# Kernel tuning notes

Measured on AMD Instinct MI355X. Metric: run time of the kernel, lower is better.

The kernel has to match this reference:

```python
import jax, jax.numpy as jnp
import numpy as np

N = 200000
MUL = 64
# e3nn normalization (irrep_normalization='component', path_normalization='element'):
# FCTP(irreps, '1x0e', irreps): per-out-irrep norm sqrt(dim)/sqrt(num_elements) * w3j(l,0,l)=1/sqrt(dim)
#   -> overall 1/sqrt(mul_in)
INV_SQRT_MUL = 1.0 / np.sqrt(MUL)        # lin0 / sc : single path, fan-in 64
INV_SQRT_2MUL = 1.0 / np.sqrt(2 * MUL)   # final lin : two mid paths feed each output irrep (fan-in 128)
INV_SQRT3 = 1.0 / np.sqrt(3.0)           # w3j(1,1,0) dot-product CG coefficient


def setup_inputs() -> dict:
    key = jax.random.key(0)
    ks = jax.random.split(key, 12)
    f = lambda k, s: jax.random.normal(k, s, dtype=jnp.float32)
    return {
        'x1': f(ks[0], (N, 4 * MUL)),          # node feats: 64x0e + 64x1o
        'edge_attr': f(ks[1], (N, 4)),         # 1x0e + 1x1o spherical harmonics
        'tp_weight': f(ks[2], (N, 4 * MUL)),   # external uvu weights, 4 paths x 64
        'node_attr': f(ks[3], (N, 1)),         # 1x0e scalar attrs
        'W_lin0_s': f(ks[4], (MUL, MUL)),
        'W_lin0_v': f(ks[5], (MUL, MUL)),
        'W_sc_s': f(ks[6], (MUL, MUL)),
        'W_sc_v': f(ks[7], (MUL, MUL)),
        'W_lin_A': f(ks[8], (MUL, MUL)),
        'W_lin_D': f(ks[9], (MUL, MUL)),
        'W_lin_B': f(ks[10], (MUL, MUL)),
        'W_lin_C': f(ks[11], (MUL, MUL)),
    }


def _fctp_scalar_attr(s, v, a, Ws, Wv, c):
    # FullyConnectedTensorProduct(mul x {0e,1o}, 1x0e, mul x {0e,1o}) with scalar attr a: [N,1]
    out_s = c * a * (s @ Ws)                                   # [N,64]
    out_v = c * a[:, :, None] * jnp.einsum('num,uw->nwm', v, Wv)  # [N,64,3]
    return out_s, out_v


def reference(x1, edge_attr, tp_weight, node_attr,
              W_lin0_s, W_lin0_v, W_sc_s, W_sc_v,
              W_lin_A, W_lin_D, W_lin_B, W_lin_C):
    n = x1.shape[0]
    s = x1[:, :MUL]                     # 64x0e
    v = x1[:, MUL:].reshape(n, MUL, 3)  # 64x1o
    a = node_attr                       # [N,1]
    e0 = edge_attr[:, :1]               # 1x0e
    e1 = edge_attr[:, 1:4]              # 1x1o

    # self-connection and input linear (both FCTP with scalar node attrs)
    sc_s, sc_v = _fctp_scalar_attr(s, v, a, W_sc_s, W_sc_v, INV_SQRT_MUL)
    s0, v0 = _fctp_scalar_attr(s, v, a, W_lin0_s, W_lin0_v, INV_SQRT_MUL)

    # uvu TensorProduct with external per-element weights; instruction order A,B,C,D
    wA = tp_weight[:, 0:MUL]
    wB = tp_weight[:, MUL:2 * MUL]
    wC = tp_weight[:, 2 * MUL:3 * MUL]
    wD = tp_weight[:, 3 * MUL:4 * MUL]
    midA = wA * s0 * e0                                              # 0e x 0e -> 0e
    midB = wB[:, :, None] * s0[:, :, None] * e1[:, None, :]         # 0e x 1o -> 1o
    midC = wC[:, :, None] * v0 * e0[:, :, None]                     # 1o x 0e -> 1o
    midD = INV_SQRT3 * wD * jnp.einsum('num,nm->nu', v0, e1)        # 1o x 1o -> 0e (dot)
    # dropout (e3nn irrep dropout) in eval mode == identity

    # final FCTP(irreps_mid, 1x0e, irreps_out): two mid paths per output irrep
    out_s = INV_SQRT_2MUL * a * (midA @ W_lin_A + midD @ W_lin_D)
    out_v = INV_SQRT_2MUL * a[:, :, None] * (
        jnp.einsum('num,uw->nwm', midB, W_lin_B)
        + jnp.einsum('num,uw->nwm', midC, W_lin_C))

    out_s = out_s + sc_s
    out_v = out_v + sc_v
    return jnp.concatenate([out_s, out_v.reshape(n, 3 * MUL)], axis=1)
```

## Files before the change

kernel.cpp:

```cpp
#include <hip/hip_runtime.h>

typedef __attribute__((ext_vector_type(4))) float f32x4;
typedef __attribute__((ext_vector_type(8))) short bf16x8;

#define MFMA(a, b, c) __builtin_amdgcn_mfma_f32_16x16x32_bf16(a, b, c, 0, 0, 0)
#define NOPS asm volatile("s_nop 7\ns_nop 7\ns_nop 7\ns_nop 7" ::: "memory")

static __device__ __forceinline__ short rnebf(float x) {
  union { float f; unsigned u; } v; v.f = x;
  return (short)((v.u + 0x7FFFu + ((v.u >> 16) & 1u)) >> 16);
}
static __device__ __forceinline__ float bf2f(short h) {
  union { unsigned u; float f; } v; v.u = ((unsigned)(unsigned short)h) << 16;
  return v.f;
}
static __device__ __forceinline__ void split2(float x, short& hi, short& lo) {
  hi = rnebf(x);
  lo = rnebf(x - bf2f(hi));
}

__global__ void prep_w(const float* __restrict__ W0, const float* __restrict__ W1,
                       const float* __restrict__ W2, const float* __restrict__ W3,
                       const float* __restrict__ W4, const float* __restrict__ W5,
                       const float* __restrict__ W6, const float* __restrict__ W7,
                       short* __restrict__ ws) {
  const float* W[8] = {W0, W1, W2, W3, W4, W5, W6, W7};
  int t = blockIdx.x * 256 + threadIdx.x;
  int lane = t & 63, fragid = (t >> 6) & 7, mat = t >> 9;
  const float* Wm = W[mat];
  int ct = fragid >> 1, kh = fragid & 1;
  int wcol = ct * 16 + (lane & 15);
  int k0 = kh * 32 + ((lane >> 4) << 3);
  bf16x8 vh, vl;
#pragma unroll
  for (int j = 0; j < 8; ++j) {
    short h, l;
    split2(Wm[(k0 + j) * 64 + wcol], h, l);
    vh[j] = h; vl[j] = l;
  }
  size_t base = ((size_t)(mat * 16) + fragid) * 512 + lane * 8;
  *(bf16x8*)(ws + base) = vh;
  *(bf16x8*)(ws + base + 4096) = vl;
}

struct BF { bf16x8 h[4][2], l[4][2]; };

static __device__ __forceinline__ void loadB(const short* __restrict__ ws, int mat, int lane,
                                             BF& B) {
#pragma unroll
  for (int ct = 0; ct < 4; ++ct)
#pragma unroll
    for (int kh = 0; kh < 2; ++kh) {
      B.h[ct][kh] = *(const bf16x8*)(ws + ((size_t)(mat * 16) + ct * 2 + kh) * 512 + lane * 8);
      B.l[ct][kh] = *(const bf16x8*)(ws + ((size_t)(mat * 16 + 8) + ct * 2 + kh) * 512 + lane * 8);
    }
}

static __device__ __forceinline__ void cluster(const bf16x8 (&ah)[2], const bf16x8 (&al)[2],
                                               const BF& B, f32x4 (&acc)[4]) {
  __builtin_amdgcn_sched_barrier(0);
#pragma unroll
  for (int ct = 0; ct < 4; ++ct)
#pragma unroll
    for (int kh = 0; kh < 2; ++kh) {
      acc[ct] = MFMA(ah[kh], B.h[ct][kh], acc[ct]);
      acc[ct] = MFMA(al[kh], B.h[ct][kh], acc[ct]);
      acc[ct] = MFMA(ah[kh], B.l[ct][kh], acc[ct]);
    }
  __builtin_amdgcn_sched_barrier(0);
  NOPS;
}

static __device__ __forceinline__ void ldM(const short* __restrict__ M, int ph, int arow,
                                           int lane, bf16x8 (&ah)[2], bf16x8 (&al)[2]) {
  int swz = (arow & 7) << 4;
#pragma unroll
  for (int kh = 0; kh < 2; ++kh) {
    int ab = (arow * 128 + kh * 64 + ((lane >> 4) << 4)) ^ swz;
    ah[kh] = *(const bf16x8*)((const char*)M + ph * 8192 + ab);
    al[kh] = *(const bf16x8*)((const char*)M + (ph + 1) * 8192 + ab);
  }
}
static __device__ __forceinline__ void stM(short* __restrict__ M, int p, int n, int w, float x) {
  short h, l;
  split2(x, h, l);
  int ab = (n * 128 + w * 2) ^ ((n & 7) << 4);
  *(short*)((char*)M + p * 8192 + ab) = h;
  *(short*)((char*)M + (p + 1) * 8192 + ab) = l;
}

__global__ __launch_bounds__(256, 2) void fused_tp(
    const float* __restrict__ x1, const float* __restrict__ edge,
    const float* __restrict__ tp, const float* __restrict__ node,
    const short* __restrict__ ws, float* __restrict__ out) {
  __shared__ short lds_s[8 * 4096];
  __shared__ float cst[64 * 6];
  const int t = threadIdx.x;
  const int R0 = blockIdx.x * 64;

  {
    int c = t;
    int plane_hi, u;
    if (c < 64) { plane_hi = 0; u = c; }
    else { int q = c - 64; u = q / 3; int m = q - u * 3; plane_hi = 2 + 2 * m; }
    char* phi = (char*)lds_s + plane_hi * 8192;
    char* plo = phi + 8192;
    const float* xc = x1 + (size_t)R0 * 256 + c;
#pragma unroll 8
    for (int i = 0; i < 64; ++i) {
      float ksc = 0.125f * node[R0 + i];
      short h, l;
      split2(ksc * xc[(size_t)i * 256], h, l);
      int ab = (i * 128 + u * 2) ^ ((i & 7) << 4);
      *(short*)(phi + ab) = h;
      *(short*)(plo + ab) = l;
    }
    if (t < 64) {
      f32x4 e = *(const f32x4*)(edge + (size_t)(R0 + t) * 4);
      float a = node[R0 + t];
      float* cr = cst + t * 6;
      cr[0] = e[0]; cr[1] = e[1]; cr[2] = e[2]; cr[3] = e[3];
      cr[4] = 0.08838834764831845f * a;
    }
  }
  __syncthreads();

  const int lane = t & 63;
  const int wid = t >> 6;
  const int r0 = wid * 16;
  const int lg = lane >> 4;
  const int arow = r0 + (lane & 15);
  const f32x4 z = {0.f, 0.f, 0.f, 0.f};

  f32x4 outS[4], outV[3][4], s0v[4], v0v[3][4];
#pragma unroll
  for (int ct = 0; ct < 4; ++ct) { outS[ct] = z; s0v[ct] = z; }
#pragma unroll
  for (int m = 0; m < 3; ++m)
#pragma unroll
    for (int ct = 0; ct < 4; ++ct) { outV[m][ct] = z; v0v[m][ct] = z; }

  {
    BF B;
    bf16x8 ah[2], al[2];
    loadB(ws, 0, lane, B);
    ldM(lds_s, 0, arow, lane, ah, al);
    cluster(ah, al, B, outS);
    loadB(ws, 1, lane, B);
    cluster(ah, al, B, s0v);
    loadB(ws, 2, lane, B);
#pragma unroll
    for (int m = 0; m < 3; ++m) {
      ldM(lds_s, 2 + 2 * m, arow, lane, ah, al);
      cluster(ah, al, B, outV[m]);
    }
    loadB(ws, 3, lane, B);
#pragma unroll
    for (int m = 0; m < 3; ++m) {
      ldM(lds_s, 2 + 2 * m, arow, lane, ah, al);
      cluster(ah, al, B, v0v[m]);
    }
  }
  __syncthreads();

#pragma unroll
  for (int reg = 0; reg < 4; ++reg) {
    int n = r0 + (lg << 2) + reg;
    const float* cr = cst + n * 6;
    float e0 = cr[0], e1x = cr[1], e1y = cr[2], e1z = cr[3], c2a = cr[4];
    const float* tr = tp + (size_t)(R0 + n) * 256;
#pragma unroll
    for (int ct = 0; ct < 4; ++ct) {
      int w = ct * 16 + (lane & 15);
      float t0 = c2a * s0v[ct][reg];
      float wa = tr[w], wb = tr[64 + w];
      stM(lds_s, 0, n, w, wa * t0 * e0);
      float bmul = wb * t0;
      stM(lds_s, 2, n, w, bmul * e1x);
      stM(lds_s, 4, n, w, bmul * e1y);
      stM(lds_s, 6, n, w, bmul * e1z);
    }
  }
  __syncthreads();

  {
    BF B;
    bf16x8 ah[2], al[2];
    loadB(ws, 4, lane, B);
    ldM(lds_s, 0, arow, lane, ah, al);
    cluster(ah, al, B, outS);
    loadB(ws, 6, lane, B);
#pragma unroll
    for (int m = 0; m < 3; ++m) {
      ldM(lds_s, 2 + 2 * m, arow, lane, ah, al);
      cluster(ah, al, B, outV[m]);
    }
  }
  __syncthreads();

#pragma unroll
  for (int reg = 0; reg < 4; ++reg) {
    int n = r0 + (lg << 2) + reg;
    const float* cr = cst + n * 6;
    float e0 = cr[0], e1x = cr[1], e1y = cr[2], e1z = cr[3], c2a = cr[4];
    const float* tr = tp + (size_t)(R0 + n) * 256;
#pragma unroll
    for (int ct = 0; ct < 4; ++ct) {
      int w = ct * 16 + (lane & 15);
      float kv0 = c2a * v0v[0][ct][reg];
      float kv1 = c2a * v0v[1][ct][reg];
      float kv2 = c2a * v0v[2][ct][reg];
      float wc = tr[128 + w], wd = tr[192 + w];
      stM(lds_s, 0, n, w, wd * (kv0 * e1x + kv1 * e1y + kv2 * e1z) * 0.5773502691896258f);
      stM(lds_s, 2, n, w, wc * kv0 * e0);
      stM(lds_s, 4, n, w, wc * kv1 * e0);
      stM(lds_s, 6, n, w, wc * kv2 * e0);
    }
  }
  __syncthreads();

  {
    BF B;
    bf16x8 ah[2], al[2];
    loadB(ws, 5, lane, B);
    ldM(lds_s, 0, arow, lane, ah, al);
    cluster(ah, al, B, outS);
    loadB(ws, 7, lane, B);
#pragma unroll
    for (int m = 0; m < 3; ++m) {
      ldM(lds_s, 2 + 2 * m, arow, lane, ah, al);
      cluster(ah, al, B, outV[m]);
    }
  }

#pragma unroll
  for (int reg = 0; reg < 4; ++reg) {
    int n = r0 + (lg << 2) + reg;
    float* orow = out + (size_t)(R0 + n) * 256;
#pragma unroll
    for (int ct = 0; ct < 4; ++ct) {
      int w = ct * 16 + (lane & 15);
      orow[w] = outS[ct][reg];
      float* vp = orow + 64 + 3 * w;
      vp[0] = outV[0][ct][reg];
      vp[1] = outV[1][ct][reg];
      vp[2] = outV[2][ct][reg];
    }
  }
}

extern "C" void kernel_launch(void* const* d_in, const int* in_sizes, int n_in,
                              void* d_out, int out_size, void* d_ws, size_t ws_size,
                              hipStream_t stream) {
  const float* x1   = (const float*)d_in[0];
  const float* edge = (const float*)d_in[1];
  const float* tp   = (const float*)d_in[2];
  const float* node = (const float*)d_in[3];
  short* ws = (short*)d_ws;
  int n = in_sizes[0] / 256;

  prep_w<<<16, 256, 0, stream>>>(
      (const float*)d_in[6], (const float*)d_in[4],
      (const float*)d_in[7], (const float*)d_in[5],
      (const float*)d_in[8], (const float*)d_in[9],
      (const float*)d_in[10], (const float*)d_in[11], ws);

  fused_tp<<<n / 64, 256, 0, stream>>>(x1, edge, tp, node, ws, (float*)d_out);
}
```

Baseline: 202.1 us.

## Split output columns across two waves per row tile with 512-thread blocks

Doubles the block to 512 threads, so each 16-row tile is handled by two waves that each compute half of the 64 output columns. Per-wave accumulator and B-fragment register footprints are halved, which could allow more waves in flight, and the initial LDS staging loop is split between the two thread halves. The cost is that every A fragment is now loaded from LDS by twice as many waves. Each wave also has shorter MFMA clusters relative to the fixed NOP padding and barrier overhead.

```diff
diff --git a/kernel.cpp b/kernel.cpp
--- a/kernel.cpp
+++ b/kernel.cpp
@@ -43,29 +43,30 @@
   *(bf16x8*)(ws + base + 4096) = vl;
 }
 
-struct BF { bf16x8 h[4][2], l[4][2]; };
+struct BF2 { bf16x8 h[2][2], l[2][2]; };
 
 static __device__ __forceinline__ void loadB(const short* __restrict__ ws, int mat, int lane,
-                                             BF& B) {
-#pragma unroll
-  for (int ct = 0; ct < 4; ++ct)
+                                             int ch, BF2& B) {
+#pragma unroll
+  for (int cti = 0; cti < 2; ++cti)
 #pragma unroll
     for (int kh = 0; kh < 2; ++kh) {
-      B.h[ct][kh] = *(const bf16x8*)(ws + ((size_t)(mat * 16) + ct * 2 + kh) * 512 + lane * 8);
-      B.l[ct][kh] = *(const bf16x8*)(ws + ((size_t)(mat * 16 + 8) + ct * 2 + kh) * 512 + lane * 8);
+      int ct = 2 * ch + cti;
+      B.h[cti][kh] = *(const bf16x8*)(ws + ((size_t)(mat * 16) + ct * 2 + kh) * 512 + lane * 8);
+      B.l[cti][kh] = *(const bf16x8*)(ws + ((size_t)(mat * 16 + 8) + ct * 2 + kh) * 512 + lane * 8);
     }
 }
 
 static __device__ __forceinline__ void cluster(const bf16x8 (&ah)[2], const bf16x8 (&al)[2],
-                                               const BF& B, f32x4 (&acc)[4]) {
+                                               const BF2& B, f32x4 (&acc)[2]) {
   __builtin_amdgcn_sched_barrier(0);
 #pragma unroll
-  for (int ct = 0; ct < 4; ++ct)
+  for (int cti = 0; cti < 2; ++cti)
 #pragma unroll
     for (int kh = 0; kh < 2; ++kh) {
-      acc[ct] = MFMA(ah[kh], B.h[ct][kh], acc[ct]);
-      acc[ct] = MFMA(al[kh], B.h[ct][kh], acc[ct]);
-      acc[ct] = MFMA(ah[kh], B.l[ct][kh], acc[ct]);
+      acc[cti] = MFMA(ah[kh], B.h[cti][kh], acc[cti]);
+      acc[cti] = MFMA(al[kh], B.h[cti][kh], acc[cti]);
+      acc[cti] = MFMA(ah[kh], B.l[cti][kh], acc[cti]);
     }
   __builtin_amdgcn_sched_barrier(0);
   NOPS;
@@ -89,7 +90,7 @@
   *(short*)((char*)M + (p + 1) * 8192 + ab) = l;
 }
 
-__global__ __launch_bounds__(256, 2) void fused_tp(
+__global__ __launch_bounds__(512, 2) void fused_tp(
     const float* __restrict__ x1, const float* __restrict__ edge,
     const float* __restrict__ tp, const float* __restrict__ node,
     const short* __restrict__ ws, float* __restrict__ out) {
@@ -97,9 +98,11 @@
   __shared__ float cst[64 * 6];
   const int t = threadIdx.x;
   const int R0 = blockIdx.x * 64;
-
-  {
-    int c = t;
+  const int lane = t & 63;
+
+  {
+    int c = t & 255;
+    int half = t >> 8;
     int plane_hi, u;
     if (c < 64) { plane_hi = 0; u = c; }
     else { int q = c - 64; u = q / 3; int m = q - u * 3; plane_hi = 2 + 2 * m; }
@@ -107,7 +110,8 @@
     char* plo = phi + 8192;
     const float* xc = x1 + (size_t)R0 * 256 + c;
 #pragma unroll 8
-    for (int i = 0; i < 64; ++i) {
+    for (int ii = 0; ii < 32; ++ii) {
+      int i = half * 32 + ii;
       float ksc = 0.125f * node[R0 + i];
       short h, l;
       split2(ksc * xc[(size_t)i * 256], h, l);
@@ -125,36 +129,36 @@
   }
   __syncthreads();
 
-  const int lane = t & 63;
   const int wid = t >> 6;
-  const int r0 = wid * 16;
+  const int ch = wid & 1;
+  const int r0 = (wid >> 1) * 16;
   const int lg = lane >> 4;
   const int arow = r0 + (lane & 15);
   const f32x4 z = {0.f, 0.f, 0.f, 0.f};
 
-  f32x4 outS[4], outV[3][4], s0v[4], v0v[3][4];
-#pragma unroll
-  for (int ct = 0; ct < 4; ++ct) { outS[ct] = z; s0v[ct] = z; }
+  f32x4 outS[2], outV[3][2], s0v[2], v0v[3][2];
+#pragma unroll
+  for (int c2 = 0; c2 < 2; ++c2) { outS[c2] = z; s0v[c2] = z; }
 #pragma unroll
   for (int m = 0; m < 3; ++m)
 #pragma unroll
-    for (int ct = 0; ct < 4; ++ct) { outV[m][ct] = z; v0v[m][ct] = z; }
-
-  {
-    BF B;
+    for (int c2 = 0; c2 < 2; ++c2) { outV[m][c2] = z; v0v[m][c2] = z; }
+
+  {
+    BF2 B;
     bf16x8 ah[2], al[2];
-    loadB(ws, 0, lane, B);
+    loadB(ws, 0, lane, ch, B);
     ldM(lds_s, 0, arow, lane, ah, al);
     cluster(ah, al, B, outS);
-    loadB(ws, 1, lane, B);
+    loadB(ws, 1, lane, ch, B);
     cluster(ah, al, B, s0v);
-    loadB(ws, 2, lane, B);
+    loadB(ws, 2, lane, ch, B);
 #pragma unroll
     for (int m = 0; m < 3; ++m) {
       ldM(lds_s, 2 + 2 * m, arow, lane, ah, al);
       cluster(ah, al, B, outV[m]);
     }
-    loadB(ws, 3, lane, B);
+    loadB(ws, 3, lane, ch, B);
 #pragma unroll
     for (int m = 0; m < 3; ++m) {
       ldM(lds_s, 2 + 2 * m, arow, lane, ah, al);
@@ -170,9 +174,9 @@
     float e0 = cr[0], e1x = cr[1], e1y = cr[2], e1z = cr[3], c2a = cr[4];
     const float* tr = tp + (size_t)(R0 + n) * 256;
 #pragma unroll
-    for (int ct = 0; ct < 4; ++ct) {
-      int w = ct * 16 + (lane & 15);
-      float t0 = c2a * s0v[ct][reg];
+    for (int cti = 0; cti < 2; ++cti) {
+      int w = (2 * ch + cti) * 16 + (lane & 15);
+      float t0 = c2a * s0v[cti][reg];
       float wa = tr[w], wb = tr[64 + w];
       stM(lds_s, 0, n, w, wa * t0 * e0);
       float bmul = wb * t0;
@@ -184,12 +188,12 @@
   __syncthreads();
 
   {
-    BF B;
+    BF2 B;
     bf16x8 ah[2], al[2];
-    loadB(ws, 4, lane, B);
+    loadB(ws, 4, lane, ch, B);
     ldM(lds_s, 0, arow, lane, ah, al);
     cluster(ah, al, B, outS);
-    loadB(ws, 6, lane, B);
+    loadB(ws, 6, lane, ch, B);
 #pragma unroll
     for (int m = 0; m < 3; ++m) {
       ldM(lds_s, 2 + 2 * m, arow, lane, ah, al);
@@ -205,11 +209,11 @@
     float e0 = cr[0], e1x = cr[1], e1y = cr[2], e1z = cr[3], c2a = cr[4];
     const float* tr = tp + (size_t)(R0 + n) * 256;
 #pragma unroll
-    for (int ct = 0; ct < 4; ++ct) {
-      int w = ct * 16 + (lane & 15);
-      float kv0 = c2a * v0v[0][ct][reg];
-      float kv1 = c2a * v0v[1][ct][reg];
-      float kv2 = c2a * v0v[2][ct][reg];
+    for (int cti = 0; cti < 2; ++cti) {
+      int w = (2 * ch + cti) * 16 + (lane & 15);
+      float kv0 = c2a * v0v[0][cti][reg];
+      float kv1 = c2a * v0v[1][cti][reg];
+      float kv2 = c2a * v0v[2][cti][reg];
       float wc = tr[128 + w], wd = tr[192 + w];
       stM(lds_s, 0, n, w, wd * (kv0 * e1x + kv1 * e1y + kv2 * e1z) * 0.5773502691896258f);
       stM(lds_s, 2, n, w, wc * kv0 * e0);
@@ -220,12 +224,12 @@
   __syncthreads();
 
   {
-    BF B;
+    BF2 B;
     bf16x8 ah[2], al[2];
-    loadB(ws, 5, lane, B);
+    loadB(ws, 5, lane, ch, B);
     ldM(lds_s, 0, arow, lane, ah, al);
     cluster(ah, al, B, outS);
-    loadB(ws, 7, lane, B);
+    loadB(ws, 7, lane, ch, B);
 #pragma unroll
     for (int m = 0; m < 3; ++m) {
       ldM(lds_s, 2 + 2 * m, arow, lane, ah, al);
@@ -238,13 +242,13 @@
     int n = r0 + (lg << 2) + reg;
     float* orow = out + (size_t)(R0 + n) * 256;
 #pragma unroll
-    for (int ct = 0; ct < 4; ++ct) {
-      int w = ct * 16 + (lane & 15);
-      orow[w] = outS[ct][reg];
+    for (int cti = 0; cti < 2; ++cti) {
+      int w = (2 * ch + cti) * 16 + (lane & 15);
+      orow[w] = outS[cti][reg];
       float* vp = orow + 64 + 3 * w;
-      vp[0] = outV[0][ct][reg];
-      vp[1] = outV[1][ct][reg];
-      vp[2] = outV[2][ct][reg];
+      vp[0] = outV[0][cti][reg];
+      vp[1] = outV[1][cti][reg];
+      vp[2] = outV[2][cti][reg];
     }
   }
 }
@@ -265,5 +269,5 @@
       (const float*)d_in[8], (const float*)d_in[9],
       (const float*)d_in[10], (const float*)d_in[11], ws);
 
-  fused_tp<<<n / 64, 256, 0, stream>>>(x1, edge, tp, node, ws, (float*)d_out);
-}
+  fused_tp<<<n / 64, 512, 0, stream>>>(x1, edge, tp, node, ws, (float*)d_out);
+}
```

New measurement: 222.9 us. +10.3%, slower.
